# Optimization experiments

Measured on AMD Instinct MI355X. Metric: run time of the kernel, lower is better.

The kernel has to match this reference:

```python
import jax, jax.numpy as jnp
import numpy as np

B, S, D, H = 2, 2048, 768, 12
DK = D // H
DF = 3072
SOFTCAP = 30.0
LN_EPS = 1e-5
NEG_INF = -1e30


def layer_norm(x, g, b):
    m = jnp.mean(x, axis=-1, keepdims=True)
    v = jnp.mean(jnp.square(x - m), axis=-1, keepdims=True)
    return (x - m) * jax.lax.rsqrt(v + LN_EPS) * g + b


def setup_inputs() -> dict:
    key = jax.random.key(0)
    ks = jax.random.split(key, 12)
    s = 0.02
    x = jax.random.normal(ks[0], (B, S, D), jnp.float32)
    count_bias = jax.random.normal(ks[1], (B, 1, S, S), jnp.float32)
    # causal mask: True = allowed
    attn_mask = jnp.broadcast_to(jnp.tril(jnp.ones((S, S), bool)), (B, 1, S, S))
    Wq = jax.random.normal(ks[2], (D, D), jnp.float32) * s
    Wk = jax.random.normal(ks[3], (D, D), jnp.float32) * s
    Wv = jax.random.normal(ks[4], (D, D), jnp.float32) * s
    Wo = jax.random.normal(ks[5], (D, D), jnp.float32) * s
    W1 = jax.random.normal(ks[6], (D, DF), jnp.float32) * s
    W2 = jax.random.normal(ks[7], (DF, D), jnp.float32) * s
    g1 = jnp.ones((D,), jnp.float32)
    b1 = jnp.zeros((D,), jnp.float32)
    g2 = jnp.ones((D,), jnp.float32)
    b2 = jnp.zeros((D,), jnp.float32)
    return dict(x=x, count_bias=count_bias, attn_mask=attn_mask, Wq=Wq, Wk=Wk,
                Wv=Wv, Wo=Wo, W1=W1, W2=W2, g1=g1, b1=b1, g2=g2, b2=b2)


def reference(x, count_bias, attn_mask, Wq, Wk, Wv, Wo, W1, W2, g1, b1, g2, b2):
    # pre-norm (note: residual taken from normed activations, faithful to source)
    h = layer_norm(x, g1, b1)                                   # (B,S,D)
    q = (h @ Wq).reshape(B, S, H, DK).transpose(0, 2, 1, 3)     # (B,H,S,DK)
    k = (h @ Wk).reshape(B, S, H, DK).transpose(0, 2, 1, 3)
    v = (h @ Wv).reshape(B, S, H, DK).transpose(0, 2, 1, 3)
    scale = 1.0 / np.sqrt(DK).astype(np.float32)
    scores = jnp.einsum('bhqd,bhkd->bhqk', q, k) * scale + count_bias
    scores = jnp.tanh(scores / SOFTCAP) * SOFTCAP               # softcap
    scores = jnp.where(attn_mask, scores, NEG_INF)
    weights = jax.nn.softmax(scores, axis=-1)
    o = jnp.einsum('bhqk,bhkd->bhqd', weights, v)               # (B,H,S,DK)
    o = o.transpose(0, 2, 1, 3).reshape(B, S, D) @ Wo
    x1 = o + h
    h2 = layer_norm(x1, g2, b2)
    ffn = jax.nn.gelu(h2 @ W1, approximate=False) @ W2
    return ffn + h2
```

## Files before the change

kernel.cpp:

```cpp
#include <hip/hip_runtime.h>
#include <hip/hip_bf16.h>
#include <cstdint>

#define Bn 2
#define Sn 2048
#define Dn 768
#define Hn 12
#define DKn 64
#define DFn 3072
#define Mrows 4096

typedef float f32x4 __attribute__((ext_vector_type(4)));
typedef __bf16 bf16x8 __attribute__((ext_vector_type(8)));
typedef short s16x8 __attribute__((ext_vector_type(8)));
typedef short s16x4 __attribute__((ext_vector_type(4)));

__device__ __forceinline__ f32x4 MFMA(s16x8 a, s16x8 b, f32x4 c) {
  return __builtin_amdgcn_mfma_f32_16x16x32_bf16(
      __builtin_bit_cast(bf16x8, a), __builtin_bit_cast(bf16x8, b), c, 0, 0, 0);
}

__device__ __forceinline__ void g2lds16(const void* g, void* l) {
  __builtin_amdgcn_global_load_lds(
      (__attribute__((address_space(1))) void*)(g),
      (__attribute__((address_space(3))) void*)(l), 16, 0, 0);
}

__device__ __forceinline__ short f2bf(float f) {
  unsigned u = __builtin_bit_cast(unsigned, f);
  unsigned r = (u + 0x7fffu + ((u >> 16) & 1u)) >> 16;
  return (short)r;
}

__device__ __forceinline__ float bf2f(short s) {
  unsigned u = ((unsigned)(unsigned short)s) << 16;
  return __builtin_bit_cast(float, u);
}

#define C1f 0.0120224586f
#define C2f 0.0961796722f
#define C3f -86.5617013f

__global__ __launch_bounds__(256) void bias_prep(const float* __restrict__ bias,
                                                 short* __restrict__ biasb) {
  int gid = blockIdx.x * 256 + threadIdx.x;
  size_t i8 = (size_t)gid * 8;
  int q = (int)((i8 >> 11) & 2047);
  int k0 = (int)(i8 & 2047);
  f32x4 v0 = *(const f32x4*)(bias + i8);
  f32x4 v1 = *(const f32x4*)(bias + i8 + 4);
  s16x8 o;
#pragma unroll
  for (int j = 0; j < 4; j++) o[j] = (k0 + j <= q) ? f2bf(v0[j] * C2f) : f2bf(-1e30f);
#pragma unroll
  for (int j = 0; j < 4; j++) o[4 + j] = (k0 + 4 + j <= q) ? f2bf(v1[j] * C2f) : f2bf(-1e30f);
  *(s16x8*)(biasb + i8) = o;
}

__global__ void wtrans(const float* __restrict__ in, short* __restrict__ out, int R, int C) {
  __shared__ float t[32][33];
  int c0 = blockIdx.x * 32, r0 = blockIdx.y * 32;
  int tx = threadIdx.x, ty = threadIdx.y;
#pragma unroll
  for (int i = 0; i < 4; i++) t[ty + i * 8][tx] = in[(size_t)(r0 + ty + i * 8) * C + c0 + tx];
  __syncthreads();
#pragma unroll
  for (int i = 0; i < 4; i++) out[(size_t)(c0 + ty + i * 8) * R + r0 + tx] = f2bf(t[tx][ty + i * 8]);
}

__global__ void wtrans3(const float* __restrict__ Wq, const float* __restrict__ Wk,
                        const float* __restrict__ Wv, short* __restrict__ out) {
  __shared__ float t[32][33];
  int z = blockIdx.z;
  const float* in = (z == 0) ? Wq : (z == 1) ? Wk : Wv;
  short* o = out + (size_t)z * Dn * Dn;
  int c0 = blockIdx.x * 32, r0 = blockIdx.y * 32;
  int tx = threadIdx.x, ty = threadIdx.y;
#pragma unroll
  for (int i = 0; i < 4; i++) t[ty + i * 8][tx] = in[(size_t)(r0 + ty + i * 8) * Dn + c0 + tx];
  __syncthreads();
#pragma unroll
  for (int i = 0; i < 4; i++) o[(size_t)(c0 + ty + i * 8) * Dn + r0 + tx] = f2bf(t[tx][ty + i * 8]);
}

__global__ __launch_bounds__(256) void ln_kernel(const float* __restrict__ x,
                                                 const float* __restrict__ g,
                                                 const float* __restrict__ b,
                                                 short* __restrict__ hb,
                                                 float* __restrict__ hf) {
  int row = blockIdx.x;
  const float* xr = x + (size_t)row * Dn;
  int tid = threadIdx.x;
  float v[3];
  float s = 0.f, ss = 0.f;
#pragma unroll
  for (int i = 0; i < 3; i++) {
    v[i] = xr[tid + i * 256];
    s += v[i];
    ss += v[i] * v[i];
  }
#pragma unroll
  for (int m = 1; m < 64; m <<= 1) {
    s += __shfl_xor(s, m);
    ss += __shfl_xor(ss, m);
  }
  __shared__ float red[8];
  int w = tid >> 6, lane = tid & 63;
  if (lane == 0) { red[w] = s; red[4 + w] = ss; }
  __syncthreads();
  s = red[0] + red[1] + red[2] + red[3];
  ss = red[4] + red[5] + red[6] + red[7];
  float mean = s * (1.0f / Dn);
  float var = ss * (1.0f / Dn) - mean * mean;
  float rs = rsqrtf(var + 1e-5f);
#pragma unroll
  for (int i = 0; i < 3; i++) {
    int c = tid + i * 256;
    float h = (v[i] - mean) * rs * g[c] + b[c];
    hb[(size_t)row * Dn + c] = f2bf(h);
    hf[(size_t)row * Dn + c] = h;
  }
}

template <int EPI>
__global__ __launch_bounds__(256) void gemm_bt(const short* __restrict__ A,
                                               const short* __restrict__ Bt,
                                               short* __restrict__ Cb,
                                               const float* __restrict__ addm,
                                               float* __restrict__ Cf,
                                               int M, int N, int K) {
  __shared__ __align__(16) short As[4096];
  __shared__ __align__(16) short Bs[4096];
  int tid = threadIdx.x;
  int lane = tid & 63, w = tid >> 6, g = lane >> 4, lt = lane & 15;
  int wr = w >> 1, wc = w & 1;
  int m0 = blockIdx.x * 128, n0 = blockIdx.y * 128;
  int r0 = tid >> 2, c4 = tid & 3;
  int cc = c4 ^ ((r0 >> 1) & 3);
  const short* Ag0 = A + (size_t)(m0 + r0) * K + cc * 8;
  const short* Ag1 = A + (size_t)(m0 + r0 + 64) * K + cc * 8;
  const short* Bg0 = Bt + (size_t)(n0 + r0) * K + cc * 8;
  const short* Bg1 = Bt + (size_t)(n0 + r0 + 64) * K + cc * 8;
  int swr = (lt >> 1) & 3;
  int cfrag = (g ^ swr) * 8;
  f32x4 acc[4][4] = {};
  for (int k0 = 0; k0 < K; k0 += 32) {
    g2lds16(Ag0 + k0, &As[tid * 8]);
    g2lds16(Ag1 + k0, &As[2048 + tid * 8]);
    g2lds16(Bg0 + k0, &Bs[tid * 8]);
    g2lds16(Bg1 + k0, &Bs[2048 + tid * 8]);
    __syncthreads();
    s16x8 af[4], bfr[4];
#pragma unroll
    for (int i = 0; i < 4; i++) {
      af[i] = *(const s16x8*)&As[(wr * 64 + i * 16 + lt) * 32 + cfrag];
      bfr[i] = *(const s16x8*)&Bs[(wc * 64 + i * 16 + lt) * 32 + cfrag];
    }
#pragma unroll
    for (int mi = 0; mi < 4; mi++)
#pragma unroll
      for (int ni = 0; ni < 4; ni++) acc[mi][ni] = MFMA(af[mi], bfr[ni], acc[mi][ni]);
    __syncthreads();
  }
#pragma unroll
  for (int mi = 0; mi < 4; mi++) {
    int m = m0 + wr * 64 + mi * 16 + g * 4;
#pragma unroll
    for (int ni = 0; ni < 4; ni++) {
      int n = n0 + wc * 64 + ni * 16 + lt;
#pragma unroll
      for (int r = 0; r < 4; r++) {
        float v = acc[mi][ni][r];
        size_t idx = (size_t)(m + r) * N + n;
        if constexpr (EPI == 0) {
          Cb[idx] = f2bf(v);
        } else if constexpr (EPI == 1) {
          float ge = 0.5f * v * (1.0f + erff(v * 0.70710678f));
          Cb[idx] = f2bf(ge);
        } else {
          Cf[idx] = v + addm[idx];
        }
      }
    }
  }
}

template <int EPI>
__global__ __launch_bounds__(256, 4) void gemm64(const short* __restrict__ A,
                                                 const short* __restrict__ Bt,
                                                 short* __restrict__ Cb,
                                                 const float* __restrict__ addm,
                                                 float* __restrict__ Cf,
                                                 int M, int N, int K) {
  __shared__ __align__(16) short As[2][4096];
  __shared__ __align__(16) short Bs[2][4096];
  int tid = threadIdx.x, lane = tid & 63, w = tid >> 6, g = lane >> 4, lt = lane & 15;
  int wr = w >> 1, wc = w & 1;
  int m0 = blockIdx.x * 64, n0 = blockIdx.y * 64;
  int r0 = tid >> 3, cc = (tid & 7) ^ (r0 & 7);
  const short* asrc0 = A + (size_t)(m0 + r0) * K + cc * 8;
  const short* asrc1 = A + (size_t)(m0 + r0 + 32) * K + cc * 8;
  const short* bsrc0 = Bt + (size_t)(n0 + r0) * K + cc * 8;
  const short* bsrc1 = Bt + (size_t)(n0 + r0 + 32) * K + cc * 8;
  int sw = lt & 7;
  int ch0 = (g ^ sw) * 8, ch1 = ((4 + g) ^ sw) * 8;
  f32x4 acc[2][2] = {};
  g2lds16(asrc0, &As[0][tid * 8]);
  g2lds16(asrc1, &As[0][2048 + tid * 8]);
  g2lds16(bsrc0, &Bs[0][tid * 8]);
  g2lds16(bsrc1, &Bs[0][2048 + tid * 8]);
  __syncthreads();
  int nsteps = K >> 6;
  for (int t = 0; t < nsteps; t++) {
    int cur = t & 1;
    if (t + 1 < nsteps) {
      int k0 = (t + 1) << 6;
      g2lds16(asrc0 + k0, &As[cur ^ 1][tid * 8]);
      g2lds16(asrc1 + k0, &As[cur ^ 1][2048 + tid * 8]);
      g2lds16(bsrc0 + k0, &Bs[cur ^ 1][tid * 8]);
      g2lds16(bsrc1 + k0, &Bs[cur ^ 1][2048 + tid * 8]);
    }
    s16x8 af[2][2], bf[2][2];
#pragma unroll
    for (int mi = 0; mi < 2; mi++) {
      af[mi][0] = *(const s16x8*)&As[cur][(wr * 32 + mi * 16 + lt) * 64 + ch0];
      af[mi][1] = *(const s16x8*)&As[cur][(wr * 32 + mi * 16 + lt) * 64 + ch1];
    }
#pragma unroll
    for (int ni = 0; ni < 2; ni++) {
      bf[ni][0] = *(const s16x8*)&Bs[cur][(wc * 32 + ni * 16 + lt) * 64 + ch0];
      bf[ni][1] = *(const s16x8*)&Bs[cur][(wc * 32 + ni * 16 + lt) * 64 + ch1];
    }
#pragma unroll
    for (int mi = 0; mi < 2; mi++)
#pragma unroll
      for (int ni = 0; ni < 2; ni++) {
        acc[mi][ni] = MFMA(af[mi][0], bf[ni][0], acc[mi][ni]);
        acc[mi][ni] = MFMA(af[mi][1], bf[ni][1], acc[mi][ni]);
      }
    __syncthreads();
  }
#pragma unroll
  for (int mi = 0; mi < 2; mi++) {
    int m = m0 + wr * 32 + mi * 16 + g * 4;
#pragma unroll
    for (int ni = 0; ni < 2; ni++) {
      int n = n0 + wc * 32 + ni * 16 + lt;
#pragma unroll
      for (int r = 0; r < 4; r++) {
        float v = acc[mi][ni][r];
        size_t idx = (size_t)(m + r) * N + n;
        if constexpr (EPI == 0) {
          Cb[idx] = f2bf(v);
        } else if constexpr (EPI == 1) {
          float ge = 0.5f * v * (1.0f + erff(v * 0.70710678f));
          Cb[idx] = f2bf(ge);
        } else {
          Cf[idx] = v + addm[idx];
        }
      }
    }
  }
}

__global__ void vtrans(const short* __restrict__ qkv, short* __restrict__ vt) {
  __shared__ short t[32][33];
  int bh = blockIdx.z;
  int b = bh / Hn, h = bh % Hn;
  int s0 = blockIdx.x * 32, d0 = blockIdx.y * 32;
  int tx = threadIdx.x, ty = threadIdx.y;
#pragma unroll
  for (int i = 0; i < 4; i++)
    t[ty + i * 8][tx] =
        qkv[(size_t)(b * Sn + s0 + ty + i * 8) * (3 * Dn) + 2 * Dn + h * DKn + d0 + tx];
  __syncthreads();
#pragma unroll
  for (int i = 0; i < 4; i++)
    vt[(size_t)(bh * DKn + d0 + ty + i * 8) * Sn + s0 + tx] = t[tx][ty + i * 8];
}

__global__ __launch_bounds__(512, 2) void attn_kernel(const short* __restrict__ qkv,
                                                      const short* __restrict__ vt,
                                                      const short* __restrict__ biasb,
                                                      short* __restrict__ o) {
  __shared__ __align__(16) short Ks[2][4096];
  __shared__ __align__(16) short Vs[2][4096];
  __shared__ __align__(16) short plds[8][16][72];
  int bh = blockIdx.x;
  int qt = 15 - (int)blockIdx.y;
  int b = bh / Hn, h = bh - b * Hn;
  int tid = threadIdx.x, w = tid >> 6, lane = tid & 63, g = lane >> 4, lt = lane & 15;
  int q0 = qt * 128 + w * 16;
  const short* qbase = qkv + (size_t)(b * Sn + q0 + lt) * (3 * Dn) + h * DKn;
  s16x8 qf0 = *(const s16x8*)(qbase + g * 8);
  s16x8 qf1 = *(const s16x8*)(qbase + 32 + g * 8);
  int srow = tid >> 3, scc = (tid & 7) ^ (srow & 7);
  const short* ksrc = qkv + (size_t)(b * Sn + srow) * (3 * Dn) + Dn + h * DKn + scc * 8;
  const short* vsrc = vt + ((size_t)bh * DKn + srow) * Sn + scc * 8;
  int sw = lt & 7;
  int ch0 = (g ^ sw) * 8, ch1 = ((4 + g) ^ sw) * 8;
  const short* bbase = biasb + ((size_t)b * Sn + q0 + g * 4) * Sn + lt;
  f32x4 oacc[4] = {};
  float lsum[4] = {0.f, 0.f, 0.f, 0.f};
  g2lds16(ksrc, &Ks[0][tid * 8]);
  g2lds16(vsrc, &Vs[0][tid * 8]);
  short sb[16];
#pragma unroll
  for (int c = 0; c < 4; c++)
#pragma unroll
    for (int r = 0; r < 4; r++) sb[c * 4 + r] = bbase[(size_t)r * Sn + c * 16];
  __syncthreads();
  int nt = 2 * qt + 2;
  for (int t = 0; t < nt; t++) {
    int cur = t & 1;
    int kc0 = t * 64;
    if (t + 1 < nt) {
      g2lds16(ksrc + (size_t)(kc0 + 64) * (3 * Dn), &Ks[cur ^ 1][tid * 8]);
      g2lds16(vsrc + kc0 + 64, &Vs[cur ^ 1][tid * 8]);
    }
    short sbn[16];
    if (t + 1 < nt) {
      int kn = kc0 + 64;
#pragma unroll
      for (int c = 0; c < 4; c++)
#pragma unroll
        for (int r = 0; r < 4; r++) sbn[c * 4 + r] = bbase[(size_t)r * Sn + kn + c * 16];
    }
    s16x8 kf[4][2];
#pragma unroll
    for (int c = 0; c < 4; c++) {
      kf[c][0] = *(const s16x8*)&Ks[cur][(c * 16 + lt) * 64 + ch0];
      kf[c][1] = *(const s16x8*)&Ks[cur][(c * 16 + lt) * 64 + ch1];
    }
    f32x4 s[4] = {};
#pragma unroll
    for (int c = 0; c < 4; c++) {
      s[c] = MFMA(qf0, kf[c][0], s[c]);
      s[c] = MFMA(qf1, kf[c][1], s[c]);
    }
    s16x8 vf[4][2];
#pragma unroll
    for (int dt = 0; dt < 4; dt++) {
      vf[dt][0] = *(const s16x8*)&Vs[cur][(dt * 16 + lt) * 64 + ch0];
      vf[dt][1] = *(const s16x8*)&Vs[cur][(dt * 16 + lt) * 64 + ch1];
    }
#pragma unroll
    for (int c = 0; c < 4; c++) {
#pragma unroll
      for (int r = 0; r < 4; r++) {
        float targ = fmaf(s[c][r], C1f, bf2f(sb[c * 4 + r]));
        float e = __builtin_amdgcn_exp2f(targ);
        float u = __builtin_amdgcn_rcpf(1.0f + e);
        float p = __builtin_amdgcn_exp2f(C3f * u);
        lsum[r] += p;
        plds[w][g * 4 + r][c * 16 + lt] = f2bf(p);
      }
    }
    s16x8 pf0 = *(const s16x8*)&plds[w][lt][g * 8];
    s16x8 pf1 = *(const s16x8*)&plds[w][lt][32 + g * 8];
#pragma unroll
    for (int dt = 0; dt < 4; dt++) {
      oacc[dt] = MFMA(pf0, vf[dt][0], oacc[dt]);
      oacc[dt] = MFMA(pf1, vf[dt][1], oacc[dt]);
    }
    __syncthreads();
    if (t + 1 < nt) {
#pragma unroll
      for (int i = 0; i < 16; i++) sb[i] = sbn[i];
    }
  }
  float inv[4];
#pragma unroll
  for (int r = 0; r < 4; r++) {
    float l = lsum[r];
    l += __shfl_xor(l, 1);
    l += __shfl_xor(l, 2);
    l += __shfl_xor(l, 4);
    l += __shfl_xor(l, 8);
    inv[r] = __builtin_amdgcn_rcpf(l);
  }
  short* obase = o + (size_t)(b * Sn + q0 + g * 4) * Dn + h * DKn + lt;
#pragma unroll
  for (int dt = 0; dt < 4; dt++)
#pragma unroll
    for (int r = 0; r < 4; r++) obase[(size_t)r * Dn + dt * 16] = f2bf(oacc[dt][r] * inv[r]);
}

extern "C" void kernel_launch(void* const* d_in, const int* in_sizes, int n_in,
                              void* d_out, int out_size, void* d_ws, size_t ws_size,
                              hipStream_t stream) {
  const float* x = (const float*)d_in[0];
  const float* bias = (const float*)d_in[1];
  const float* Wq = (const float*)d_in[3];
  const float* Wk = (const float*)d_in[4];
  const float* Wv = (const float*)d_in[5];
  const float* Wo = (const float*)d_in[6];
  const float* W1 = (const float*)d_in[7];
  const float* W2 = (const float*)d_in[8];
  const float* g1 = (const float*)d_in[9];
  const float* b1 = (const float*)d_in[10];
  const float* g2 = (const float*)d_in[11];
  const float* b2 = (const float*)d_in[12];
  float* out = (float*)d_out;
  char* ws = (char*)d_ws;

  short* wqkv_t = (short*)(ws + 0);
  short* wo_t = (short*)(ws + 3538944);
  short* w1_t = (short*)(ws + 4718592);
  short* w2_t = (short*)(ws + 9437184);
  short* hb = (short*)(ws + 14155776);
  float* hf = (float*)(ws + 20447232);
  short* qkv = (short*)(ws + 33030144);
  short* a1 = qkv;
  short* vt = (short*)(ws + 58195968);
  float* x1 = (float*)(ws + 58195968);
  short* o_ = (short*)(ws + 70778880);
  short* biasb = (short*)(ws + 77070336);
  short* h2b = hb;
  float* h2f = hf;

  dim3 tb(32, 8);
  bias_prep<<<4096, 256, 0, stream>>>(bias, biasb);
  wtrans3<<<dim3(24, 24, 3), tb, 0, stream>>>(Wq, Wk, Wv, wqkv_t);
  wtrans<<<dim3(24, 24), tb, 0, stream>>>(Wo, wo_t, Dn, Dn);
  wtrans<<<dim3(96, 24), tb, 0, stream>>>(W1, w1_t, Dn, DFn);
  wtrans<<<dim3(24, 96), tb, 0, stream>>>(W2, w2_t, DFn, Dn);

  ln_kernel<<<Mrows, 256, 0, stream>>>(x, g1, b1, hb, hf);

  gemm_bt<0><<<dim3(32, 18), 256, 0, stream>>>(hb, wqkv_t, qkv, nullptr, nullptr,
                                               Mrows, 3 * Dn, Dn);
  vtrans<<<dim3(64, 2, Bn * Hn), tb, 0, stream>>>(qkv, vt);
  attn_kernel<<<dim3(24, 16), 512, 0, stream>>>(qkv, vt, biasb, o_);

  gemm64<2><<<dim3(64, 12), 256, 0, stream>>>(o_, wo_t, nullptr, hf, x1,
                                              Mrows, Dn, Dn);
  ln_kernel<<<Mrows, 256, 0, stream>>>(x1, g2, b2, h2b, h2f);
  gemm_bt<1><<<dim3(32, 24), 256, 0, stream>>>(h2b, w1_t, a1, nullptr, nullptr,
                                               Mrows, DFn, Dn);
  gemm64<2><<<dim3(64, 12), 256, 0, stream>>>(a1, w2_t, nullptr, h2f, out,
                                              Mrows, Dn, DFn);
}
```

Before: 339.0 us.

## Split-K output and FFN-down GEMMs, fuse partial reduction into LN, rebalance attention

The Wo and W2 projections now run through the 128x128 gemm_bt kernel with a 4-way split over K. Each slice writes bf16 partials into reused workspace buffers, and the separate 64x64 gemm64 kernel is removed. The partials are summed together with the fp32 residual inside a new fused LayerNorm kernel and a vectorised final-add kernel. Attention moves to 64-row query tiles with 256 threads, and tiles are ordered so that heavy and light causal tiles are interleaved, which improves load balance and occupancy. In exchange, storing partials in bf16 costs precision, and the partial buffers add memory traffic.

```diff
diff --git a/kernel.cpp b/kernel.cpp
--- a/kernel.cpp
+++ b/kernel.cpp
@@ -122,29 +122,103 @@
   }
 }
 
+__global__ __launch_bounds__(256) void ln_fuse4(const short* __restrict__ p0,
+                                                const short* __restrict__ p1,
+                                                const short* __restrict__ p2,
+                                                const short* __restrict__ p3,
+                                                const float* __restrict__ hfin,
+                                                const float* __restrict__ g,
+                                                const float* __restrict__ b,
+                                                short* __restrict__ hb,
+                                                float* __restrict__ hfout) {
+  int row = blockIdx.x;
+  size_t base = (size_t)row * Dn;
+  int tid = threadIdx.x;
+  float v[3];
+  float s = 0.f, ss = 0.f;
+#pragma unroll
+  for (int i = 0; i < 3; i++) {
+    size_t idx = base + tid + i * 256;
+    float x = bf2f(p0[idx]) + bf2f(p1[idx]) + bf2f(p2[idx]) + bf2f(p3[idx]) + hfin[idx];
+    v[i] = x;
+    s += x;
+    ss += x * x;
+  }
+#pragma unroll
+  for (int m = 1; m < 64; m <<= 1) {
+    s += __shfl_xor(s, m);
+    ss += __shfl_xor(ss, m);
+  }
+  __shared__ float red[8];
+  int w = tid >> 6, lane = tid & 63;
+  if (lane == 0) { red[w] = s; red[4 + w] = ss; }
+  __syncthreads();
+  s = red[0] + red[1] + red[2] + red[3];
+  ss = red[4] + red[5] + red[6] + red[7];
+  float mean = s * (1.0f / Dn);
+  float var = ss * (1.0f / Dn) - mean * mean;
+  float rs = rsqrtf(var + 1e-5f);
+#pragma unroll
+  for (int i = 0; i < 3; i++) {
+    int c = tid + i * 256;
+    float h = (v[i] - mean) * rs * g[c] + b[c];
+    hb[base + c] = f2bf(h);
+    hfout[base + c] = h;
+  }
+}
+
+__global__ __launch_bounds__(256) void final_add(const short* __restrict__ q0,
+                                                 const short* __restrict__ q1,
+                                                 const short* __restrict__ q2,
+                                                 const short* __restrict__ q3,
+                                                 const float* __restrict__ h2f,
+                                                 float* __restrict__ out) {
+  size_t i8 = ((size_t)blockIdx.x * 256 + threadIdx.x) * 8;
+  s16x8 a = *(const s16x8*)(q0 + i8);
+  s16x8 b = *(const s16x8*)(q1 + i8);
+  s16x8 c = *(const s16x8*)(q2 + i8);
+  s16x8 d = *(const s16x8*)(q3 + i8);
+  f32x4 h0 = *(const f32x4*)(h2f + i8);
+  f32x4 h1 = *(const f32x4*)(h2f + i8 + 4);
+  f32x4 o0, o1;
+#pragma unroll
+  for (int j = 0; j < 4; j++)
+    o0[j] = bf2f(a[j]) + bf2f(b[j]) + bf2f(c[j]) + bf2f(d[j]) + h0[j];
+#pragma unroll
+  for (int j = 0; j < 4; j++)
+    o1[j] = bf2f(a[4 + j]) + bf2f(b[4 + j]) + bf2f(c[4 + j]) + bf2f(d[4 + j]) + h1[j];
+  *(f32x4*)(out + i8) = o0;
+  *(f32x4*)(out + i8 + 4) = o1;
+}
+
 template <int EPI>
 __global__ __launch_bounds__(256) void gemm_bt(const short* __restrict__ A,
                                                const short* __restrict__ Bt,
-                                               short* __restrict__ Cb,
-                                               const float* __restrict__ addm,
-                                               float* __restrict__ Cf,
-                                               int M, int N, int K) {
+                                               short* __restrict__ c0p,
+                                               short* __restrict__ c1p,
+                                               short* __restrict__ c2p,
+                                               short* __restrict__ c3p,
+                                               int M, int N, int Kspan, int lda) {
   __shared__ __align__(16) short As[4096];
   __shared__ __align__(16) short Bs[4096];
+  int z = blockIdx.z;
+  const short* Ab = A + (size_t)z * Kspan;
+  const short* Bb = Bt + (size_t)z * Kspan;
+  short* Cb = (z == 0) ? c0p : (z == 1) ? c1p : (z == 2) ? c2p : c3p;
   int tid = threadIdx.x;
   int lane = tid & 63, w = tid >> 6, g = lane >> 4, lt = lane & 15;
   int wr = w >> 1, wc = w & 1;
   int m0 = blockIdx.x * 128, n0 = blockIdx.y * 128;
   int r0 = tid >> 2, c4 = tid & 3;
   int cc = c4 ^ ((r0 >> 1) & 3);
-  const short* Ag0 = A + (size_t)(m0 + r0) * K + cc * 8;
-  const short* Ag1 = A + (size_t)(m0 + r0 + 64) * K + cc * 8;
-  const short* Bg0 = Bt + (size_t)(n0 + r0) * K + cc * 8;
-  const short* Bg1 = Bt + (size_t)(n0 + r0 + 64) * K + cc * 8;
+  const short* Ag0 = Ab + (size_t)(m0 + r0) * lda + cc * 8;
+  const short* Ag1 = Ab + (size_t)(m0 + r0 + 64) * lda + cc * 8;
+  const short* Bg0 = Bb + (size_t)(n0 + r0) * lda + cc * 8;
+  const short* Bg1 = Bb + (size_t)(n0 + r0 + 64) * lda + cc * 8;
   int swr = (lt >> 1) & 3;
   int cfrag = (g ^ swr) * 8;
   f32x4 acc[4][4] = {};
-  for (int k0 = 0; k0 < K; k0 += 32) {
+  for (int k0 = 0; k0 < Kspan; k0 += 32) {
     g2lds16(Ag0 + k0, &As[tid * 8]);
     g2lds16(Ag1 + k0, &As[2048 + tid * 8]);
     g2lds16(Bg0 + k0, &Bs[tid * 8]);
@@ -174,89 +248,9 @@
         size_t idx = (size_t)(m + r) * N + n;
         if constexpr (EPI == 0) {
           Cb[idx] = f2bf(v);
-        } else if constexpr (EPI == 1) {
+        } else {
           float ge = 0.5f * v * (1.0f + erff(v * 0.70710678f));
           Cb[idx] = f2bf(ge);
-        } else {
-          Cf[idx] = v + addm[idx];
-        }
-      }
-    }
-  }
-}
-
-template <int EPI>
-__global__ __launch_bounds__(256, 4) void gemm64(const short* __restrict__ A,
-                                                 const short* __restrict__ Bt,
-                                                 short* __restrict__ Cb,
-                                                 const float* __restrict__ addm,
-                                                 float* __restrict__ Cf,
-                                                 int M, int N, int K) {
-  __shared__ __align__(16) short As[2][4096];
-  __shared__ __align__(16) short Bs[2][4096];
-  int tid = threadIdx.x, lane = tid & 63, w = tid >> 6, g = lane >> 4, lt = lane & 15;
-  int wr = w >> 1, wc = w & 1;
-  int m0 = blockIdx.x * 64, n0 = blockIdx.y * 64;
-  int r0 = tid >> 3, cc = (tid & 7) ^ (r0 & 7);
-  const short* asrc0 = A + (size_t)(m0 + r0) * K + cc * 8;
-  const short* asrc1 = A + (size_t)(m0 + r0 + 32) * K + cc * 8;
-  const short* bsrc0 = Bt + (size_t)(n0 + r0) * K + cc * 8;
-  const short* bsrc1 = Bt + (size_t)(n0 + r0 + 32) * K + cc * 8;
-  int sw = lt & 7;
-  int ch0 = (g ^ sw) * 8, ch1 = ((4 + g) ^ sw) * 8;
-  f32x4 acc[2][2] = {};
-  g2lds16(asrc0, &As[0][tid * 8]);
-  g2lds16(asrc1, &As[0][2048 + tid * 8]);
-  g2lds16(bsrc0, &Bs[0][tid * 8]);
-  g2lds16(bsrc1, &Bs[0][2048 + tid * 8]);
-  __syncthreads();
-  int nsteps = K >> 6;
-  for (int t = 0; t < nsteps; t++) {
-    int cur = t & 1;
-    if (t + 1 < nsteps) {
-      int k0 = (t + 1) << 6;
-      g2lds16(asrc0 + k0, &As[cur ^ 1][tid * 8]);
-      g2lds16(asrc1 + k0, &As[cur ^ 1][2048 + tid * 8]);
-      g2lds16(bsrc0 + k0, &Bs[cur ^ 1][tid * 8]);
-      g2lds16(bsrc1 + k0, &Bs[cur ^ 1][2048 + tid * 8]);
-    }
-    s16x8 af[2][2], bf[2][2];
-#pragma unroll
-    for (int mi = 0; mi < 2; mi++) {
-      af[mi][0] = *(const s16x8*)&As[cur][(wr * 32 + mi * 16 + lt) * 64 + ch0];
-      af[mi][1] = *(const s16x8*)&As[cur][(wr * 32 + mi * 16 + lt) * 64 + ch1];
-    }
-#pragma unroll
-    for (int ni = 0; ni < 2; ni++) {
-      bf[ni][0] = *(const s16x8*)&Bs[cur][(wc * 32 + ni * 16 + lt) * 64 + ch0];
-      bf[ni][1] = *(const s16x8*)&Bs[cur][(wc * 32 + ni * 16 + lt) * 64 + ch1];
-    }
-#pragma unroll
-    for (int mi = 0; mi < 2; mi++)
-#pragma unroll
-      for (int ni = 0; ni < 2; ni++) {
-        acc[mi][ni] = MFMA(af[mi][0], bf[ni][0], acc[mi][ni]);
-        acc[mi][ni] = MFMA(af[mi][1], bf[ni][1], acc[mi][ni]);
-      }
-    __syncthreads();
-  }
-#pragma unroll
-  for (int mi = 0; mi < 2; mi++) {
-    int m = m0 + wr * 32 + mi * 16 + g * 4;
-#pragma unroll
-    for (int ni = 0; ni < 2; ni++) {
-      int n = n0 + wc * 32 + ni * 16 + lt;
-#pragma unroll
-      for (int r = 0; r < 4; r++) {
-        float v = acc[mi][ni][r];
-        size_t idx = (size_t)(m + r) * N + n;
-        if constexpr (EPI == 0) {
-          Cb[idx] = f2bf(v);
-        } else if constexpr (EPI == 1) {
-          float ge = 0.5f * v * (1.0f + erff(v * 0.70710678f));
-          Cb[idx] = f2bf(ge);
-        } else {
-          Cf[idx] = v + addm[idx];
         }
       }
     }
@@ -279,47 +273,56 @@
     vt[(size_t)(bh * DKn + d0 + ty + i * 8) * Sn + s0 + tx] = t[tx][ty + i * 8];
 }
 
-__global__ __launch_bounds__(512, 2) void attn_kernel(const short* __restrict__ qkv,
+__global__ __launch_bounds__(256, 3) void attn_kernel(const short* __restrict__ qkv,
                                                       const short* __restrict__ vt,
                                                       const short* __restrict__ biasb,
                                                       short* __restrict__ o) {
   __shared__ __align__(16) short Ks[2][4096];
   __shared__ __align__(16) short Vs[2][4096];
-  __shared__ __align__(16) short plds[8][16][72];
+  __shared__ __align__(16) short plds[4][16][72];
   int bh = blockIdx.x;
-  int qt = 15 - (int)blockIdx.y;
+  int by = blockIdx.y;
+  int qt = (by & 1) ? (31 - (by >> 1)) : (by >> 1);
   int b = bh / Hn, h = bh - b * Hn;
   int tid = threadIdx.x, w = tid >> 6, lane = tid & 63, g = lane >> 4, lt = lane & 15;
-  int q0 = qt * 128 + w * 16;
+  int q0 = qt * 64 + w * 16;
   const short* qbase = qkv + (size_t)(b * Sn + q0 + lt) * (3 * Dn) + h * DKn;
   s16x8 qf0 = *(const s16x8*)(qbase + g * 8);
   s16x8 qf1 = *(const s16x8*)(qbase + 32 + g * 8);
-  int srow = tid >> 3, scc = (tid & 7) ^ (srow & 7);
-  const short* ksrc = qkv + (size_t)(b * Sn + srow) * (3 * Dn) + Dn + h * DKn + scc * 8;
-  const short* vsrc = vt + ((size_t)bh * DKn + srow) * Sn + scc * 8;
+  int sr0 = tid >> 3, scc = (tid & 7) ^ (sr0 & 7);
+  const short* kseg = qkv + (size_t)b * Sn * (3 * Dn) + Dn + h * DKn;
+  const short* ksrc0 = kseg + (size_t)sr0 * (3 * Dn) + scc * 8;
+  const short* ksrc1 = kseg + (size_t)(sr0 + 32) * (3 * Dn) + scc * 8;
+  const short* vseg = vt + (size_t)bh * DKn * Sn;
+  const short* vsrc0 = vseg + (size_t)sr0 * Sn + scc * 8;
+  const short* vsrc1 = vseg + (size_t)(sr0 + 32) * Sn + scc * 8;
   int sw = lt & 7;
   int ch0 = (g ^ sw) * 8, ch1 = ((4 + g) ^ sw) * 8;
   const short* bbase = biasb + ((size_t)b * Sn + q0 + g * 4) * Sn + lt;
   f32x4 oacc[4] = {};
   float lsum[4] = {0.f, 0.f, 0.f, 0.f};
-  g2lds16(ksrc, &Ks[0][tid * 8]);
-  g2lds16(vsrc, &Vs[0][tid * 8]);
+  g2lds16(ksrc0, &Ks[0][tid * 8]);
+  g2lds16(ksrc1, &Ks[0][2048 + tid * 8]);
+  g2lds16(vsrc0, &Vs[0][tid * 8]);
+  g2lds16(vsrc1, &Vs[0][2048 + tid * 8]);
   short sb[16];
 #pragma unroll
   for (int c = 0; c < 4; c++)
 #pragma unroll
     for (int r = 0; r < 4; r++) sb[c * 4 + r] = bbase[(size_t)r * Sn + c * 16];
   __syncthreads();
-  int nt = 2 * qt + 2;
-  for (int t = 0; t < nt; t++) {
+  for (int t = 0; t <= qt; t++) {
     int cur = t & 1;
     int kc0 = t * 64;
-    if (t + 1 < nt) {
-      g2lds16(ksrc + (size_t)(kc0 + 64) * (3 * Dn), &Ks[cur ^ 1][tid * 8]);
-      g2lds16(vsrc + kc0 + 64, &Vs[cur ^ 1][tid * 8]);
+    if (t < qt) {
+      size_t koff = (size_t)(kc0 + 64) * (3 * Dn);
+      g2lds16(ksrc0 + koff, &Ks[cur ^ 1][tid * 8]);
+      g2lds16(ksrc1 + koff, &Ks[cur ^ 1][2048 + tid * 8]);
+      g2lds16(vsrc0 + kc0 + 64, &Vs[cur ^ 1][tid * 8]);
+      g2lds16(vsrc1 + kc0 + 64, &Vs[cur ^ 1][2048 + tid * 8]);
     }
     short sbn[16];
-    if (t + 1 < nt) {
+    if (t < qt) {
       int kn = kc0 + 64;
 #pragma unroll
       for (int c = 0; c < 4; c++)
@@ -364,7 +367,7 @@
       oacc[dt] = MFMA(pf1, vf[dt][1], oacc[dt]);
     }
     __syncthreads();
-    if (t + 1 < nt) {
+    if (t < qt) {
 #pragma unroll
       for (int i = 0; i < 16; i++) sb[i] = sbn[i];
     }
@@ -413,11 +416,16 @@
   short* qkv = (short*)(ws + 33030144);
   short* a1 = qkv;
   short* vt = (short*)(ws + 58195968);
-  float* x1 = (float*)(ws + 58195968);
   short* o_ = (short*)(ws + 70778880);
   short* biasb = (short*)(ws + 77070336);
   short* h2b = hb;
   float* h2f = hf;
+  const int PSZ = Mrows * Dn;
+  short* pW = qkv;
+  short* pF0 = vt;
+  short* pF1 = vt + PSZ;
+  short* pF2 = o_;
+  short* pF3 = biasb;
 
   dim3 tb(32, 8);
   bias_prep<<<4096, 256, 0, stream>>>(bias, biasb);
@@ -428,16 +436,18 @@
 
   ln_kernel<<<Mrows, 256, 0, stream>>>(x, g1, b1, hb, hf);
 
-  gemm_bt<0><<<dim3(32, 18), 256, 0, stream>>>(hb, wqkv_t, qkv, nullptr, nullptr,
-                                               Mrows, 3 * Dn, Dn);
+  gemm_bt<0><<<dim3(32, 18, 1), 256, 0, stream>>>(hb, wqkv_t, qkv, qkv, qkv, qkv,
+                                                  Mrows, 3 * Dn, Dn, Dn);
   vtrans<<<dim3(64, 2, Bn * Hn), tb, 0, stream>>>(qkv, vt);
-  attn_kernel<<<dim3(24, 16), 512, 0, stream>>>(qkv, vt, biasb, o_);
-
-  gemm64<2><<<dim3(64, 12), 256, 0, stream>>>(o_, wo_t, nullptr, hf, x1,
-                                              Mrows, Dn, Dn);
-  ln_kernel<<<Mrows, 256, 0, stream>>>(x1, g2, b2, h2b, h2f);
-  gemm_bt<1><<<dim3(32, 24), 256, 0, stream>>>(h2b, w1_t, a1, nullptr, nullptr,
-                                               Mrows, DFn, Dn);
-  gemm64<2><<<dim3(64, 12), 256, 0, stream>>>(a1, w2_t, nullptr, h2f, out,
-                                              Mrows, Dn, DFn);
-}
+  attn_kernel<<<dim3(24, 32), 256, 0, stream>>>(qkv, vt, biasb, o_);
+
+  gemm_bt<0><<<dim3(32, 6, 4), 256, 0, stream>>>(o_, wo_t, pW, pW + PSZ, pW + 2 * PSZ,
+                                                 pW + 3 * PSZ, Mrows, Dn, 192, Dn);
+  ln_fuse4<<<Mrows, 256, 0, stream>>>(pW, pW + PSZ, pW + 2 * PSZ, pW + 3 * PSZ,
+                                      hf, g2, b2, h2b, h2f);
+  gemm_bt<1><<<dim3(32, 24, 1), 256, 0, stream>>>(h2b, w1_t, a1, a1, a1, a1,
+                                                  Mrows, DFn, Dn, Dn);
+  gemm_bt<0><<<dim3(32, 6, 4), 256, 0, stream>>>(a1, w2_t, pF0, pF1, pF2, pF3,
+                                                 Mrows, Dn, 768, DFn);
+  final_add<<<1536, 256, 0, stream>>>(pF0, pF1, pF2, pF3, h2f, out);
+}
```

Result: no change. 336.9 us (-0.6%).
